# Performance work log

Measured on AMD Instinct MI355X. Metric: run time of the kernel, lower is better.

Reference implementation:

```python
import jax, jax.numpy as jnp
import numpy as np

D_EMBED = 32


def setup_inputs() -> dict:
    key = jax.random.key(0)
    ks = jax.random.split(key, 10)
    B, N, D = 16, 16384, D_EMBED
    s = 1.0 / np.sqrt(D)
    return {
        "h_pos": jax.random.normal(ks[0], (B, N, D), dtype=jnp.float32),
        "h_geo": jax.random.normal(ks[1], (B, N, D), dtype=jnp.float32),
        "n_clusters": 128,
        "Wq": jax.random.uniform(ks[2], (D, D), jnp.float32, -s, s),
        "bq": jax.random.uniform(ks[3], (D,), jnp.float32, -s, s),
        "Wk": jax.random.uniform(ks[4], (D, D), jnp.float32, -s, s),
        "bk": jax.random.uniform(ks[5], (D,), jnp.float32, -s, s),
        "Wv": jax.random.uniform(ks[6], (D, D), jnp.float32, -s, s),
        "bv": jax.random.uniform(ks[7], (D,), jnp.float32, -s, s),
        "Wo": jax.random.uniform(ks[8], (D, D), jnp.float32, -s, s),
        "bo": jax.random.uniform(ks[9], (D,), jnp.float32, -s, s),
    }


def reference(h_pos, h_geo, n_clusters, Wq, bq, Wk, bk, Wv, bv, Wo, bo):
    B, N, D = h_pos.shape
    C = n_clusters
    S = N // C  # cluster size (contiguous equal-size kmeans clusters)
    # Linear projections (torch Linear: x @ W^T + b)
    Q = h_geo @ Wq.T + bq
    K = h_geo @ Wk.T + bk
    V = h_pos @ Wv.T + bv
    # group points into clusters: [B, C, S, D]
    Qc = Q.reshape(B, C, S, D) * (1.0 / jnp.sqrt(jnp.asarray(D, Q.dtype)))
    Kc = K.reshape(B, C, S, D)
    Vc = V.reshape(B, C, S, D)
    # per-cluster attention: softmax(Q_c K_c^T) V_c
    scores = jnp.einsum("bcsd,bctd->bcst", Qc, Kc)  # [B, C, S, S]
    attn = jax.nn.softmax(scores, axis=-1)
    out = jnp.einsum("bcst,bctd->bcsd", attn, Vc).reshape(B, N, D)
    return out @ Wo.T + bo
```

## Files before the change

### kernel.cpp

```cpp
#include <hip/hip_runtime.h>

typedef __attribute__((ext_vector_type(4))) float  f32x4;
typedef __attribute__((ext_vector_type(8))) short  s16x8;

static __device__ __forceinline__ short f2bf(float x) {
    union { __bf16 b; short s; } u; u.b = (__bf16)x;
    return u.s;
}

static __device__ __forceinline__ s16x8 load_frag_f32(const float* __restrict__ base,
                                                      int stride, int row, int k0) {
    const float* p = base + (size_t)row * stride + k0;
    f32x4 a = *(const f32x4*)p;
    f32x4 b = *(const f32x4*)(p + 4);
    s16x8 f;
    f[0]=f2bf(a[0]); f[1]=f2bf(a[1]); f[2]=f2bf(a[2]); f[3]=f2bf(a[3]);
    f[4]=f2bf(b[0]); f[5]=f2bf(b[1]); f[6]=f2bf(b[2]); f[7]=f2bf(b[3]);
    return f;
}

#define MFMA(a,b,c) __builtin_amdgcn_mfma_f32_16x16x32_bf16((a),(b),(c),0,0,0)

#define GSCALE 0.25503164217809464f

__global__ __launch_bounds__(256, 3) void dlsa_kernel(
    const float* __restrict__ h_pos, const float* __restrict__ h_geo,
    const float* __restrict__ Wq, const float* __restrict__ bq,
    const float* __restrict__ Wk,
    const float* __restrict__ Wv, const float* __restrict__ bv,
    const float* __restrict__ Wo, const float* __restrict__ bo,
    float* __restrict__ out)
{
    constexpr int D = 32, S = 128, NN = 16384, XS = 40;

    __shared__ __align__(16) short buf[20480];
    short* sVt = buf;
    short* sP  = buf + 4096;
    short* sXp = sP;
    float* cbuf = (float*)(buf + 9216);

    const int tid = threadIdx.x;
    const int wv  = tid >> 6;
    const int ln  = tid & 63;
    const int lr  = ln & 15;
    const int lg  = ln >> 4;
    const int lk  = lg << 3;
    const int r0  = wv * 32;

    short* gsl = buf + 9472 + wv * 1088;
    short* wsl = gsl + 1024;

    const int blk = blockIdx.x;
    const int b   = blk >> 7;
    const int c   = blk & 127;
    const float* xg = h_geo + (size_t)(b * NN + c * S) * D;
    const float* xp = h_pos + (size_t)(b * NN + c * S) * D;
    float* outp = out + (size_t)(b * NN + c * S) * D;

    s16x8 aXg[2], aXp[2];
#pragma unroll
    for (int mi = 0; mi < 2; ++mi) {
        aXg[mi] = load_frag_f32(xg, D, r0 + mi * 16 + lr, lk);
        aXp[mi] = load_frag_f32(xp, D, r0 + mi * 16 + lr, lk);
    }

    const f32x4 z4 = {0.f, 0.f, 0.f, 0.f};

    s16x8 aWq[2], bWk[2], a_bq;
#pragma unroll
    for (int ni = 0; ni < 2; ++ni) {
#pragma unroll
        for (int j = 0; j < 8; ++j) {
            aWq[ni][j] = f2bf(Wq[(lk + j) * 32 + ni * 16 + lr]);
            bWk[ni][j] = f2bf(Wk[(lk + j) * 32 + ni * 16 + lr]);
        }
    }
    {
        f32x4 q0 = *(const f32x4*)&bq[lk];
        f32x4 q1 = *(const f32x4*)&bq[lk + 4];
#pragma unroll
        for (int j = 0; j < 4; ++j) { a_bq[j] = f2bf(q0[j]); a_bq[4 + j] = f2bf(q1[j]); }
    }
#pragma unroll
    for (int ni = 0; ni < 2; ++ni)
#pragma unroll
        for (int kt = 0; kt < 2; ++kt) {
            f32x4 g = MFMA(aWq[ni], bWk[kt], z4);
#pragma unroll
            for (int r = 0; r < 4; ++r)
                gsl[(ni * 16 + lg * 4 + r) * 32 + kt * 16 + lr] = f2bf(g[r] * GSCALE);
        }
#pragma unroll
    for (int kt = 0; kt < 2; ++kt) {
        f32x4 w4 = MFMA(a_bq, bWk[kt], z4);
        if (lg == 0) wsl[kt * 16 + lr] = f2bf(w4[0] * GSCALE);
    }
    s16x8 fG[2];
#pragma unroll
    for (int ni = 0; ni < 2; ++ni)
        fG[ni] = *(const s16x8*)&gsl[(ni * 16 + lr) * 32 + lk];
    s16x8 wf = *(const s16x8*)&wsl[lk];
    if (lr != 0) {
#pragma unroll
        for (int i = 0; i < 8; ++i) wf[i] = 0;
    }

    s16x8 fWv[2], fWo[2];
    float vbv[2], vbo[2];
#pragma unroll
    for (int ni = 0; ni < 2; ++ni) {
        int n = ni * 16 + lr;
        fWv[ni] = load_frag_f32(Wv, 32, n, lk);
        fWo[ni] = load_frag_f32(Wo, 32, n, lk);
        vbv[ni] = bv[n]; vbo[ni] = bo[n];
    }

#pragma unroll
    for (int mi = 0; mi < 2; ++mi) {
        f32x4 cc = MFMA(aXg[mi], wf, z4);
        if (lr == 0) {
#pragma unroll
            for (int r = 0; r < 4; ++r) cbuf[r0 + mi * 16 + lg * 4 + r] = cc[r];
        }
#pragma unroll
        for (int ni = 0; ni < 2; ++ni) {
            f32x4 xq = MFMA(aXg[mi], fG[ni], z4);
            f32x4 vv = MFMA(aXp[mi], fWv[ni], z4);
            int row = r0 + mi * 16 + lg * 4;
            int col = ni * 16 + lr;
#pragma unroll
            for (int r = 0; r < 4; ++r)
                sXp[(row + r) * XS + col] = f2bf(xq[r]);
#pragma unroll
            for (int r = 0; r < 4; ++r) {
                int uc = lg * 4 + r;
                int ul = wv * 2 + mi;
                sVt[col * 128 + ((uc ^ (col & 15)) << 3) + ul] = f2bf(vv[r] + vbv[ni]);
            }
        }
    }
    __syncthreads();

    float cv[8];
#pragma unroll
    for (int nt = 0; nt < 8; ++nt) cv[nt] = cbuf[nt * 16 + lr];

    f32x4 sc[2][8];
#pragma unroll
    for (int nt = 0; nt < 8; ++nt) {
        s16x8 xb = *(const s16x8*)&sXp[(nt * 16 + lr) * XS + lk];
        f32x4 cb = { cv[nt], cv[nt], cv[nt], cv[nt] };
        sc[0][nt] = MFMA(aXg[0], xb, cb);
        sc[1][nt] = MFMA(aXg[1], xb, cb);
    }
    __syncthreads();

    float inv_[2][4];
#pragma unroll
    for (int mi = 0; mi < 2; ++mi) {
#pragma unroll
        for (int r = 0; r < 4; ++r) {
            float p[8]; float s = 0.f;
#pragma unroll
            for (int nt = 0; nt < 8; ++nt) {
                p[nt] = __builtin_amdgcn_exp2f(sc[mi][nt][r]);
                s += p[nt];
            }
            s += __shfl_xor(s, 1);
            s += __shfl_xor(s, 2);
            s += __shfl_xor(s, 4);
            s += __shfl_xor(s, 8);
            inv_[mi][r] = __builtin_amdgcn_rcpf(s);
            s16x8 pk;
#pragma unroll
            for (int nt = 0; nt < 8; ++nt) pk[nt] = f2bf(p[nt]);
            int row = r0 + mi * 16 + lg * 4 + r;
            *(s16x8*)&sP[row * 128 + ((lr ^ (row & 15)) << 3)] = pk;
        }
    }

    f32x4 accO[2][2] = {{z4, z4}, {z4, z4}};
#pragma unroll
    for (int kt = 0; kt < 4; ++kt) {
        int ch = kt * 4 + lg;
        s16x8 pa0 = *(const s16x8*)&sP[(r0 + lr) * 128      + ((ch ^ lr) << 3)];
        s16x8 pa1 = *(const s16x8*)&sP[(r0 + 16 + lr) * 128 + ((ch ^ lr) << 3)];
        s16x8 vb0 = *(const s16x8*)&sVt[lr * 128        + ((ch ^ lr) << 3)];
        s16x8 vb1 = *(const s16x8*)&sVt[(16 + lr) * 128 + ((ch ^ lr) << 3)];
        accO[0][0] = MFMA(pa0, vb0, accO[0][0]);
        accO[0][1] = MFMA(pa0, vb1, accO[0][1]);
        accO[1][0] = MFMA(pa1, vb0, accO[1][0]);
        accO[1][1] = MFMA(pa1, vb1, accO[1][1]);
    }

    short* sO = sP + r0 * 128;
#pragma unroll
    for (int mi = 0; mi < 2; ++mi)
#pragma unroll
        for (int ni = 0; ni < 2; ++ni) {
            int row = mi * 16 + lg * 4;
            int col = ni * 16 + lr;
#pragma unroll
            for (int r = 0; r < 4; ++r)
                sO[(row + r) * XS + col] = f2bf(accO[mi][ni][r] * inv_[mi][r]);
        }
    s16x8 aO0 = *(const s16x8*)&sO[lr * XS + lk];
    s16x8 aO1 = *(const s16x8*)&sO[(16 + lr) * XS + lk];

    float* slabf = (float*)(sP + r0 * 128);
#pragma unroll
    for (int mi = 0; mi < 2; ++mi) {
        s16x8 aO = mi ? aO1 : aO0;
#pragma unroll
        for (int ni = 0; ni < 2; ++ni) {
            f32x4 y = MFMA(aO, fWo[ni], z4);
            int rl  = mi * 16 + lg * 4;
            int col = ni * 16 + lr;
            int c4  = col >> 2;
#pragma unroll
            for (int r = 0; r < 4; ++r) {
                int xc = c4 ^ ((rl + r) & 7);
                slabf[(rl + r) * 32 + (xc << 2) + (col & 3)] = y[r] + vbo[ni];
            }
        }
    }
#pragma unroll
    for (int s4 = 0; s4 < 4; ++s4) {
        int rl  = s4 * 8 + (ln >> 3);
        int chv = ln & 7;
        int xc  = chv ^ (rl & 7);
        f32x4 v = *(const f32x4*)&slabf[rl * 32 + (xc << 2)];
        *(f32x4*)&outp[(size_t)(r0 + rl) * D + chv * 4] = v;
    }
}

extern "C" void kernel_launch(void* const* d_in, const int* in_sizes, int n_in,
                              void* d_out, int out_size, void* d_ws, size_t ws_size,
                              hipStream_t stream) {
    const float* h_pos = (const float*)d_in[0];
    const float* h_geo = (const float*)d_in[1];
    const float* Wq = (const float*)d_in[3];
    const float* bq = (const float*)d_in[4];
    const float* Wk = (const float*)d_in[5];
    const float* Wv = (const float*)d_in[7];
    const float* bv = (const float*)d_in[8];
    const float* Wo = (const float*)d_in[9];
    const float* bo = (const float*)d_in[10];

    dlsa_kernel<<<dim3(2048), dim3(256), 0, stream>>>(
        h_pos, h_geo, Wq, bq, Wk, Wv, bv, Wo, bo, (float*)d_out);
}
```

Baseline: 29.86 us.

## Process two clusters per block and prefetch the next cluster's inputs

```diff
diff --git a/kernel.cpp b/kernel.cpp
--- a/kernel.cpp
+++ b/kernel.cpp
@@ -50,20 +50,6 @@
     short* gsl = buf + 9472 + wv * 1088;
     short* wsl = gsl + 1024;
 
-    const int blk = blockIdx.x;
-    const int b   = blk >> 7;
-    const int c   = blk & 127;
-    const float* xg = h_geo + (size_t)(b * NN + c * S) * D;
-    const float* xp = h_pos + (size_t)(b * NN + c * S) * D;
-    float* outp = out + (size_t)(b * NN + c * S) * D;
-
-    s16x8 aXg[2], aXp[2];
-#pragma unroll
-    for (int mi = 0; mi < 2; ++mi) {
-        aXg[mi] = load_frag_f32(xg, D, r0 + mi * 16 + lr, lk);
-        aXp[mi] = load_frag_f32(xp, D, r0 + mi * 16 + lr, lk);
-    }
-
     const f32x4 z4 = {0.f, 0.f, 0.f, 0.f};
 
     s16x8 aWq[2], bWk[2], a_bq;
@@ -104,7 +90,6 @@
 #pragma unroll
         for (int i = 0; i < 8; ++i) wf[i] = 0;
     }
-
     s16x8 fWv[2], fWo[2];
     float vbv[2], vbo[2];
 #pragma unroll
@@ -115,122 +100,166 @@
         vbv[ni] = bv[n]; vbo[ni] = bo[n];
     }
 
-#pragma unroll
-    for (int mi = 0; mi < 2; ++mi) {
-        f32x4 cc = MFMA(aXg[mi], wf, z4);
-        if (lr == 0) {
-#pragma unroll
-            for (int r = 0; r < 4; ++r) cbuf[r0 + mi * 16 + lg * 4 + r] = cc[r];
-        }
-#pragma unroll
-        for (int ni = 0; ni < 2; ++ni) {
-            f32x4 xq = MFMA(aXg[mi], fG[ni], z4);
-            f32x4 vv = MFMA(aXp[mi], fWv[ni], z4);
-            int row = r0 + mi * 16 + lg * 4;
-            int col = ni * 16 + lr;
-#pragma unroll
-            for (int r = 0; r < 4; ++r)
-                sXp[(row + r) * XS + col] = f2bf(xq[r]);
+    int cl0 = blockIdx.x * 2;
+    s16x8 aXg[2], aXp[2];
+    {
+        const float* xg = h_geo + (size_t)cl0 * S * D;
+        const float* xp = h_pos + (size_t)cl0 * S * D;
+#pragma unroll
+        for (int mi = 0; mi < 2; ++mi) {
+            aXg[mi] = load_frag_f32(xg, D, r0 + mi * 16 + lr, lk);
+            aXp[mi] = load_frag_f32(xp, D, r0 + mi * 16 + lr, lk);
+        }
+    }
+
+#pragma unroll
+    for (int it = 0; it < 2; ++it) {
+        const int cl = cl0 + it;
+        float* outp = out + (size_t)cl * S * D;
+        if (it) __syncthreads();
+
+#pragma unroll
+        for (int mi = 0; mi < 2; ++mi) {
+            f32x4 cc = MFMA(aXg[mi], wf, z4);
+            if (lr == 0) {
+#pragma unroll
+                for (int r = 0; r < 4; ++r) cbuf[r0 + mi * 16 + lg * 4 + r] = cc[r];
+            }
+#pragma unroll
+            for (int ni = 0; ni < 2; ++ni) {
+                f32x4 xq = MFMA(aXg[mi], fG[ni], z4);
+                f32x4 vv = MFMA(aXp[mi], fWv[ni], z4);
+                int row = r0 + mi * 16 + lg * 4;
+                int col = ni * 16 + lr;
+#pragma unroll
+                for (int r = 0; r < 4; ++r)
+                    sXp[(row + r) * XS + col] = f2bf(xq[r]);
+#pragma unroll
+                for (int r = 0; r < 4; ++r) {
+                    int uc = lg * 4 + r;
+                    int ul = wv * 2 + mi;
+                    sVt[col * 128 + ((uc ^ (col & 15)) << 3) + ul] = f2bf(vv[r] + vbv[ni]);
+                }
+            }
+        }
+        __syncthreads();
+
+        float cv[8];
+#pragma unroll
+        for (int nt = 0; nt < 8; ++nt) cv[nt] = cbuf[nt * 16 + lr];
+
+        f32x4 sc[2][8];
+#pragma unroll
+        for (int nt = 0; nt < 8; ++nt) {
+            s16x8 xb = *(const s16x8*)&sXp[(nt * 16 + lr) * XS + lk];
+            f32x4 cb = { cv[nt], cv[nt], cv[nt], cv[nt] };
+            sc[0][nt] = MFMA(aXg[0], xb, cb);
+            sc[1][nt] = MFMA(aXg[1], xb, cb);
+        }
+        __syncthreads();
+
+        f32x4 ng[4], np[4];
+        if (it == 0) {
+            const float* xg2 = h_geo + (size_t)(cl0 + 1) * S * D;
+            const float* xp2 = h_pos + (size_t)(cl0 + 1) * S * D;
+#pragma unroll
+            for (int mi = 0; mi < 2; ++mi) {
+                const float* pg = xg2 + (size_t)(r0 + mi * 16 + lr) * D + lk;
+                const float* pp = xp2 + (size_t)(r0 + mi * 16 + lr) * D + lk;
+                ng[2*mi] = *(const f32x4*)pg;  ng[2*mi+1] = *(const f32x4*)(pg + 4);
+                np[2*mi] = *(const f32x4*)pp;  np[2*mi+1] = *(const f32x4*)(pp + 4);
+            }
+        }
+
+        float inv_[2][4];
+#pragma unroll
+        for (int mi = 0; mi < 2; ++mi) {
 #pragma unroll
             for (int r = 0; r < 4; ++r) {
-                int uc = lg * 4 + r;
-                int ul = wv * 2 + mi;
-                sVt[col * 128 + ((uc ^ (col & 15)) << 3) + ul] = f2bf(vv[r] + vbv[ni]);
-            }
-        }
-    }
-    __syncthreads();
-
-    float cv[8];
-#pragma unroll
-    for (int nt = 0; nt < 8; ++nt) cv[nt] = cbuf[nt * 16 + lr];
-
-    f32x4 sc[2][8];
-#pragma unroll
-    for (int nt = 0; nt < 8; ++nt) {
-        s16x8 xb = *(const s16x8*)&sXp[(nt * 16 + lr) * XS + lk];
-        f32x4 cb = { cv[nt], cv[nt], cv[nt], cv[nt] };
-        sc[0][nt] = MFMA(aXg[0], xb, cb);
-        sc[1][nt] = MFMA(aXg[1], xb, cb);
-    }
-    __syncthreads();
-
-    float inv_[2][4];
-#pragma unroll
-    for (int mi = 0; mi < 2; ++mi) {
-#pragma unroll
-        for (int r = 0; r < 4; ++r) {
-            float p[8]; float s = 0.f;
-#pragma unroll
-            for (int nt = 0; nt < 8; ++nt) {
-                p[nt] = __builtin_amdgcn_exp2f(sc[mi][nt][r]);
-                s += p[nt];
-            }
-            s += __shfl_xor(s, 1);
-            s += __shfl_xor(s, 2);
-            s += __shfl_xor(s, 4);
-            s += __shfl_xor(s, 8);
-            inv_[mi][r] = __builtin_amdgcn_rcpf(s);
-            s16x8 pk;
-#pragma unroll
-            for (int nt = 0; nt < 8; ++nt) pk[nt] = f2bf(p[nt]);
-            int row = r0 + mi * 16 + lg * 4 + r;
-            *(s16x8*)&sP[row * 128 + ((lr ^ (row & 15)) << 3)] = pk;
-        }
-    }
-
-    f32x4 accO[2][2] = {{z4, z4}, {z4, z4}};
-#pragma unroll
-    for (int kt = 0; kt < 4; ++kt) {
-        int ch = kt * 4 + lg;
-        s16x8 pa0 = *(const s16x8*)&sP[(r0 + lr) * 128      + ((ch ^ lr) << 3)];
-        s16x8 pa1 = *(const s16x8*)&sP[(r0 + 16 + lr) * 128 + ((ch ^ lr) << 3)];
-        s16x8 vb0 = *(const s16x8*)&sVt[lr * 128        + ((ch ^ lr) << 3)];
-        s16x8 vb1 = *(const s16x8*)&sVt[(16 + lr) * 128 + ((ch ^ lr) << 3)];
-        accO[0][0] = MFMA(pa0, vb0, accO[0][0]);
-        accO[0][1] = MFMA(pa0, vb1, accO[0][1]);
-        accO[1][0] = MFMA(pa1, vb0, accO[1][0]);
-        accO[1][1] = MFMA(pa1, vb1, accO[1][1]);
-    }
-
-    short* sO = sP + r0 * 128;
-#pragma unroll
-    for (int mi = 0; mi < 2; ++mi)
-#pragma unroll
-        for (int ni = 0; ni < 2; ++ni) {
-            int row = mi * 16 + lg * 4;
-            int col = ni * 16 + lr;
-#pragma unroll
-            for (int r = 0; r < 4; ++r)
-                sO[(row + r) * XS + col] = f2bf(accO[mi][ni][r] * inv_[mi][r]);
-        }
-    s16x8 aO0 = *(const s16x8*)&sO[lr * XS + lk];
-    s16x8 aO1 = *(const s16x8*)&sO[(16 + lr) * XS + lk];
-
-    float* slabf = (float*)(sP + r0 * 128);
-#pragma unroll
-    for (int mi = 0; mi < 2; ++mi) {
-        s16x8 aO = mi ? aO1 : aO0;
-#pragma unroll
-        for (int ni = 0; ni < 2; ++ni) {
-            f32x4 y = MFMA(aO, fWo[ni], z4);
-            int rl  = mi * 16 + lg * 4;
-            int col = ni * 16 + lr;
-            int c4  = col >> 2;
-#pragma unroll
-            for (int r = 0; r < 4; ++r) {
-                int xc = c4 ^ ((rl + r) & 7);
-                slabf[(rl + r) * 32 + (xc << 2) + (col & 3)] = y[r] + vbo[ni];
-            }
-        }
-    }
-#pragma unroll
-    for (int s4 = 0; s4 < 4; ++s4) {
-        int rl  = s4 * 8 + (ln >> 3);
-        int chv = ln & 7;
-        int xc  = chv ^ (rl & 7);
-        f32x4 v = *(const f32x4*)&slabf[rl * 32 + (xc << 2)];
-        *(f32x4*)&outp[(size_t)(r0 + rl) * D + chv * 4] = v;
+                float p[8]; float s = 0.f;
+#pragma unroll
+                for (int nt = 0; nt < 8; ++nt) {
+                    p[nt] = __builtin_amdgcn_exp2f(sc[mi][nt][r]);
+                    s += p[nt];
+                }
+                s += __shfl_xor(s, 1);
+                s += __shfl_xor(s, 2);
+                s += __shfl_xor(s, 4);
+                s += __shfl_xor(s, 8);
+                inv_[mi][r] = __builtin_amdgcn_rcpf(s);
+                s16x8 pk;
+#pragma unroll
+                for (int nt = 0; nt < 8; ++nt) pk[nt] = f2bf(p[nt]);
+                int row = r0 + mi * 16 + lg * 4 + r;
+                *(s16x8*)&sP[row * 128 + ((lr ^ (row & 15)) << 3)] = pk;
+            }
+        }
+
+        f32x4 accO[2][2] = {{z4, z4}, {z4, z4}};
+#pragma unroll
+        for (int kt = 0; kt < 4; ++kt) {
+            int ch = kt * 4 + lg;
+            s16x8 pa0 = *(const s16x8*)&sP[(r0 + lr) * 128      + ((ch ^ lr) << 3)];
+            s16x8 pa1 = *(const s16x8*)&sP[(r0 + 16 + lr) * 128 + ((ch ^ lr) << 3)];
+            s16x8 vb0 = *(const s16x8*)&sVt[lr * 128        + ((ch ^ lr) << 3)];
+            s16x8 vb1 = *(const s16x8*)&sVt[(16 + lr) * 128 + ((ch ^ lr) << 3)];
+            accO[0][0] = MFMA(pa0, vb0, accO[0][0]);
+            accO[0][1] = MFMA(pa0, vb1, accO[0][1]);
+            accO[1][0] = MFMA(pa1, vb0, accO[1][0]);
+            accO[1][1] = MFMA(pa1, vb1, accO[1][1]);
+        }
+
+        short* sO = sP + r0 * 128;
+#pragma unroll
+        for (int mi = 0; mi < 2; ++mi)
+#pragma unroll
+            for (int ni = 0; ni < 2; ++ni) {
+                int row = mi * 16 + lg * 4;
+                int col = ni * 16 + lr;
+#pragma unroll
+                for (int r = 0; r < 4; ++r)
+                    sO[(row + r) * XS + col] = f2bf(accO[mi][ni][r] * inv_[mi][r]);
+            }
+        s16x8 aO0 = *(const s16x8*)&sO[lr * XS + lk];
+        s16x8 aO1 = *(const s16x8*)&sO[(16 + lr) * XS + lk];
+
+        float* slabf = (float*)(sP + r0 * 128);
+#pragma unroll
+        for (int mi = 0; mi < 2; ++mi) {
+            s16x8 aO = mi ? aO1 : aO0;
+#pragma unroll
+            for (int ni = 0; ni < 2; ++ni) {
+                f32x4 y = MFMA(aO, fWo[ni], z4);
+                int rl  = mi * 16 + lg * 4;
+                int col = ni * 16 + lr;
+                int c4  = col >> 2;
+#pragma unroll
+                for (int r = 0; r < 4; ++r) {
+                    int xc = c4 ^ ((rl + r) & 7);
+                    slabf[(rl + r) * 32 + (xc << 2) + (col & 3)] = y[r] + vbo[ni];
+                }
+            }
+        }
+#pragma unroll
+        for (int s4 = 0; s4 < 4; ++s4) {
+            int rl  = s4 * 8 + (ln >> 3);
+            int chv = ln & 7;
+            int xc  = chv ^ (rl & 7);
+            f32x4 v = *(const f32x4*)&slabf[rl * 32 + (xc << 2)];
+            *(f32x4*)&outp[(size_t)(r0 + rl) * D + chv * 4] = v;
+        }
+
+        if (it == 0) {
+#pragma unroll
+            for (int mi = 0; mi < 2; ++mi)
+#pragma unroll
+                for (int j = 0; j < 4; ++j) {
+                    aXg[mi][j]     = f2bf(ng[2*mi][j]);
+                    aXg[mi][4 + j] = f2bf(ng[2*mi+1][j]);
+                    aXp[mi][j]     = f2bf(np[2*mi][j]);
+                    aXp[mi][4 + j] = f2bf(np[2*mi+1][j]);
+                }
+        }
     }
 }
 
@@ -247,6 +276,6 @@
     const float* Wo = (const float*)d_in[9];
     const float* bo = (const float*)d_in[10];
 
-    dlsa_kernel<<<dim3(2048), dim3(256), 0, stream>>>(
+    dlsa_kernel<<<dim3(1024), dim3(256), 0, stream>>>(
         h_pos, h_geo, Wq, bq, Wk, Wv, bv, Wo, bo, (float*)d_out);
 }
```

Measured after the change: 29.31 us. About the same (-1.8%).
